# Kernel optimization log

Measured on AMD Instinct MI355X. Metric: run time of the kernel, lower is better.

Reference implementation:

```python
import jax, jax.numpy as jnp
import numpy as np

SIZE, NC, BITS = 16, 3, 8
NV = NC * BITS * SIZE * SIZE  # 6144
NH = NV
N = 32
K_LS = 32   # fixed cap on T=0 local-search Gibbs sweeps (converged rows are fixed points)
K_CP = 16   # fixed cap on coupling MH iterations (converged rows masked out)


def float2bit(x, bits=BITS):
    # quantize [0,1) floats to `bits` binary planes, as in float2bit(...).flatten(1)
    q = jnp.clip(jnp.floor(x * (2 ** bits)), 0, 2 ** bits - 1).astype(jnp.int32)
    shifts = jnp.arange(bits, dtype=jnp.int32)
    b = (q[..., None] >> shifts) & 1  # [N,nc,H,W,bits]
    return b.astype(jnp.float32)


def energy(params, v, h0, h1):
    W0, W1, b0, b1, b2 = params
    e = -jnp.sum(v * b0, axis=1)
    e = e - jnp.sum(h0 * (v @ W0.T + b1), axis=1)
    e = e - jnp.sum(h1 * (h0 @ W1.T + b2), axis=1)
    return e


def _samp(logits, r, T):
    if T == 0:
        return (logits >= 0).astype(jnp.float32)
    return (r < jax.nn.sigmoid(logits / T)).astype(jnp.float32)


def gibbs_step(params, v, h0, h1, even, fix_v, T, key):
    W0, W1, b0, b1, b2 = params
    if T == 0:
        rv = rh0 = rh1 = None
    else:
        kv, k0, k1 = jax.random.split(key, 3)
        rv = jax.random.uniform(kv, v.shape)
        rh0 = jax.random.uniform(k0, h0.shape)
        rh1 = jax.random.uniform(k1, h1.shape)
    # 'even' sweep order: v -> odd h layers -> even h layers
    v_e = v if fix_v else _samp(h0 @ W0 + b0, rv, T)
    h1_e = _samp(h0 @ W1.T + b2, rh1, T)
    h0_e = _samp(v_e @ W0.T + b1 + h1_e @ W1, rh0, T)
    # 'odd' sweep order: even h layers -> v -> odd h layers
    h0_o = _samp(v @ W0.T + b1 + h1 @ W1, rh0, T)
    v_o = v if fix_v else _samp(h0_o @ W0 + b0, rv, T)
    h1_o = _samp(h0_o @ W1.T + b2, rh1, T)
    m = even[:, None]
    return (jnp.where(m, v_e, v_o), jnp.where(m, h0_e, h0_o), jnp.where(m, h1_e, h1_o))


def local_search(params, v, h0, h1, fix_v, key):
    # T=0 deterministic descent with a fixed per-row even/odd split (rand_u drawn once);
    # converged rows are fixed points of the map, so running a fixed K_LS sweeps over the
    # full batch is equivalent to the torch masked while-loop (up to the iteration cap).
    even = jax.random.uniform(key, (v.shape[0],)) < 0.5
    def body(i, s):
        return gibbs_step(params, s[0], s[1], s[2], even, fix_v, 0, None)
    return jax.lax.fori_loop(0, K_LS, body, (v, h0, h1))


def mh_step(params, v, h0, h1, fix_v, key):
    kv, k0, k1, ku = jax.random.split(key, 4)
    v_p = v if fix_v else (jax.random.uniform(kv, v.shape) < 0.5).astype(jnp.float32)
    h0_p = (jax.random.uniform(k0, h0.shape) < 0.5).astype(jnp.float32)
    h1_p = (jax.random.uniform(k1, h1.shape) < 0.5).astype(jnp.float32)
    log_ratio = energy(params, v, h0, h1) - energy(params, v_p, h0_p, h1_p)
    acc = jax.random.uniform(ku, (v.shape[0],)) < jnp.exp(jnp.minimum(log_ratio, 0.0))
    a = acc[:, None]
    return (v if fix_v else jnp.where(a, v_p, v), jnp.where(a, h0_p, h0), jnp.where(a, h1_p, h1))


def _conv_mask(v_new, h0_new, h1_new, v, h0, h1, fix_v):
    c = jnp.ones(v.shape[0], bool) if fix_v else jnp.all(v_new == v, axis=1)
    return c & jnp.all(h0_new == h0, axis=1) & jnp.all(h1_new == h1, axis=1)


def coupling(params, v, h0, h1, fix_v, key):
    k0, key = jax.random.split(key)
    v1, h01, h11 = mh_step(params, v, h0, h1, fix_v, k0)
    e = energy(params, v1, h01, h11)
    conv = _conv_mask(v1, h01, h11, v, h0, h1, fix_v)
    def body(state, k):
        v, h0, h1, e, conv = state
        v2, h02, h12 = mh_step(params, v, h0, h1, fix_v, k)
        de = energy(params, v2, h02, h12) - energy(params, v, h0, h1)
        m = ~conv
        e = e + jnp.where(m, de, 0.0)
        conv2 = _conv_mask(v2, h02, h12, v, h0, h1, fix_v)
        mm = m[:, None]
        v = jnp.where(mm, v2, v)
        h0 = jnp.where(mm, h02, h0)
        h1 = jnp.where(mm, h12, h1)
        return (v, h0, h1, e, conv | conv2), None
    keys = jax.random.split(key, K_CP)
    (v, h0, h1, e, conv), _ = jax.lax.scan(body, (v1, h01, h11, e, conv), keys)
    return e, v, h0, h1


def _dbm_loss(v_img, W0, W1, b0, b1, b2):
    params = (W0, W1, b0, b1, b2)
    n = v_img.shape[0]
    ks = jax.random.split(jax.random.key(42), 13)
    v = float2bit(v_img).reshape(n, -1)
    # positive phase (visibles clamped, fix_v=True)
    h0 = (jax.random.uniform(ks[0], (n, NH)) < 0.5).astype(jnp.float32)
    h1 = (jax.random.uniform(ks[1], (n, NH)) < 0.5).astype(jnp.float32)
    v, h0, h1 = local_search(params, v, h0, h1, True, ks[2])
    even = jax.random.uniform(ks[3], (n,)) < 0.5
    v, h0, h1 = gibbs_step(params, v, h0, h1, even, True, 1, ks[4])
    e_pos, v, h0, h1 = coupling(params, v, h0, h1, True, ks[5])
    # negative phase (free-running)
    v = (jax.random.uniform(ks[6], v.shape) < 0.5).astype(jnp.float32)
    h0 = (jax.random.uniform(ks[7], (n, NH)) < 0.5).astype(jnp.float32)
    h1 = (jax.random.uniform(ks[8], (n, NH)) < 0.5).astype(jnp.float32)
    v, h0, h1 = local_search(params, v, h0, h1, False, ks[9])
    even = jax.random.uniform(ks[10], (n,)) < 0.5
    v, h0, h1 = gibbs_step(params, v, h0, h1, even, False, 1, ks[11])
    e_neg, v, h0, h1 = coupling(params, v, h0, h1, False, ks[12])
    return e_pos - e_neg  # [N]


def setup_inputs() -> dict:
    key = jax.random.key(0)
    kv, kw0, kw1 = jax.random.split(key, 3)
    v = jax.random.uniform(kv, (N, NC, SIZE, SIZE), dtype=jnp.float32)
    # orthogonal-like scale (unit-norm rows): entries ~ 1/sqrt(fan_in)
    W0 = jax.random.normal(kw0, (NH, NV), dtype=jnp.float32) / np.sqrt(NV)
    W1 = jax.random.normal(kw1, (NH, NH), dtype=jnp.float32) / np.sqrt(NH)
    b0 = jnp.zeros((NV,), jnp.float32)
    b1 = jnp.zeros((NH,), jnp.float32)
    b2 = jnp.zeros((NH,), jnp.float32)
    return {"v": v, "W0": W0, "W1": W1, "b0": b0, "b1": b1, "b2": b2}


def reference(v, W0, W1, b0, b1, b2):
    return _dbm_loss(v, W0, W1, b0, b1, b2)
```

## Files before the change

### kernel.cpp

```cpp
#include <hip/hip_runtime.h>
#include <cstdint>
#include <math.h>

typedef unsigned int u32;
typedef unsigned long long u64;
typedef double d4 __attribute__((ext_vector_type(4)));

#define TF_PARTITIONABLE 1

#define NU 6144
#define NB 32
#define NTOT (NU * NB)
#define NWORD 96
#define NCH 8
#define CHK 768
#define NT_TILES 24
#define HALF_BIG 98304u
#define HALF_SMALL 16u

struct Key { u32 a, b; };
struct UVec { float u[NB]; };

__host__ __device__ __forceinline__ void tf2x32(u32 k0, u32 k1, u32 x0, u32 x1, u32& o0, u32& o1) {
  const u32 k2 = k0 ^ k1 ^ 0x1BD11BDAu;
#define TFR(r) { x0 += x1; x1 = (x1 << r) | (x1 >> (32 - r)); x1 ^= x0; }
  x0 += k0; x1 += k1;
  TFR(13) TFR(15) TFR(26) TFR(6)  x0 += k1; x1 += k2 + 1u;
  TFR(17) TFR(29) TFR(16) TFR(24) x0 += k2; x1 += k0 + 2u;
  TFR(13) TFR(15) TFR(26) TFR(6)  x0 += k0; x1 += k1 + 3u;
  TFR(17) TFR(29) TFR(16) TFR(24) x0 += k1; x1 += k2 + 4u;
  TFR(13) TFR(15) TFR(26) TFR(6)  x0 += k2; x1 += k0 + 5u;
#undef TFR
  o0 = x0; o1 = x1;
}

__host__ __device__ __forceinline__ u32 rbits(u32 k0, u32 k1, u32 t, u32 half) {
#if TF_PARTITIONABLE
  (void)half;
  u32 a, b; tf2x32(k0, k1, 0u, t, a, b); return a ^ b;
#else
  u32 a, b;
  if (t < half) { tf2x32(k0, k1, t, half + t, a, b); return a; }
  tf2x32(k0, k1, t - half, t, a, b); return b;
#endif
}

__host__ __device__ __forceinline__ float u01f(u32 bits) {
  union { u32 u; float f; } c; c.u = (bits >> 9) | 0x3f800000u;
  return c.f - 1.0f;
}

__device__ __forceinline__ double pav(int probe, int l) {
  return probe ? (double)(((l * 13 + 5) & 63) + 1) : (double)(l + 1);
}
__device__ __forceinline__ double pbv(int probe, int l) {
  return probe ? (double)(((l * 11 + 2) & 63) + 1) : (double)(((l * 7 + 3) & 63) + 1);
}

__global__ __launch_bounds__(64) void k_calib(int* __restrict__ tbl) {
  int L = threadIdx.x;
  d4 z = {0.0, 0.0, 0.0, 0.0};
  d4 o0 = __builtin_amdgcn_mfma_f64_16x16x4f64(pav(0, L), pbv(0, L), z, 0, 0, 0);
  d4 o1 = __builtin_amdgcn_mfma_f64_16x16x4f64(pav(1, L), pbv(1, L), z, 0, 0, 0);
  int q = L >> 4, m16 = L & 15;
  int best = -1;
  for (int combo = 0; combo < 16; ++combo) {
    int fa = combo & 1, fb = (combo >> 1) & 1, fd = combo >> 2;
    int ok = 1;
    for (int probe = 0; probe < 2; ++probe) {
#pragma unroll
      for (int r = 0; r < 4; ++r) {
        int i, j;
        if (fd == 0)      { j = m16; i = 4 * q + r; }
        else if (fd == 1) { j = m16; i = q + 4 * r; }
        else if (fd == 2) { i = m16; j = 4 * q + r; }
        else              { i = m16; j = q + 4 * r; }
        double pred = 0.0;
#pragma unroll
        for (int k = 0; k < 4; ++k) {
          int la = fa ? (i * 4 + k) : (k * 16 + i);
          int lb = fb ? (j * 4 + k) : (k * 16 + j);
          pred += pav(probe, la) * pbv(probe, lb);
        }
        double obs = probe ? (r == 0 ? o1[0] : r == 1 ? o1[1] : r == 2 ? o1[2] : o1[3])
                           : (r == 0 ? o0[0] : r == 1 ? o0[1] : r == 2 ? o0[2] : o0[3]);
        if (pred != obs) ok = 0;
      }
    }
    if (__all(ok) && best < 0) best = combo;
  }
  int mA = 0, kA = 0, nB = 0, kB = 0, b0_ = 0, bs = 0, j0 = 0, js = 0, okf = 0;
  if (best >= 0) {
    int fa = best & 1, fb = (best >> 1) & 1, fd = best >> 2;
    if (fa) { mA = L >> 2; kA = L & 3; } else { mA = m16; kA = q; }
    if (fb) { nB = L >> 2; kB = L & 3; } else { nB = m16; kB = q; }
    if (fd == 0)      { j0 = m16; js = 0; b0_ = 4 * q; bs = 1; }
    else if (fd == 1) { j0 = m16; js = 0; b0_ = q; bs = 4; }
    else if (fd == 2) { b0_ = m16; bs = 0; j0 = 4 * q; js = 1; }
    else              { b0_ = m16; bs = 0; j0 = q; js = 4; }
    okf = 1;
  }
  int* p = tbl + L * 16;
  p[0] = mA; p[1] = kA; p[2] = nB; p[3] = kB;
  p[4] = b0_; p[5] = bs; p[6] = j0; p[7] = js; p[8] = okf;
}

__global__ void k_init(u32* __restrict__ flag, u32* __restrict__ chg) { *flag = 0u; *chg = 0u; }

__global__ void k_conv(u32* __restrict__ flag, u32* __restrict__ chg) {
  if (*flag == 0u && *chg == 0u) *flag = 1u;
  *chg = 0u;
}

__global__ void k_allconv(const u32* __restrict__ conv, u32* __restrict__ skipc) {
  if (*skipc) return;
  u32 all = 1u;
  for (int b = 0; b < NB; ++b) all &= conv[b];
  if (all) *skipc = 1u;
}

__global__ __launch_bounds__(256) void k_pos_v(const float* __restrict__ vin,
                                               double* __restrict__ xf, u64* __restrict__ pk) {
  int tid = blockIdx.x * 256 + threadIdx.x;
  int b = tid / 768, p = tid % 768;
  float x = vin[tid];
  int q = (int)floorf(x * 256.0f);
  q = q < 0 ? 0 : (q > 255 ? 255 : q);
  ((unsigned char*)pk)[b * 768 + p] = (unsigned char)q;
  int ubase = p * 8;
#pragma unroll
  for (int bit = 0; bit < 8; ++bit)
    xf[(size_t)(ubase + bit) * NB + b] = (double)((q >> bit) & 1);
}

__global__ __launch_bounds__(256) void k_bern(u32 k0, u32 k1,
                                              double* __restrict__ xf, u64* __restrict__ pk,
                                              const u32* __restrict__ skip) {
  if (skip && *skip) return;
  int tid = blockIdx.x * 256 + threadIdx.x;
  int b = tid / NU, j = tid % NU;
  float u = u01f(rbits(k0, k1, (u32)tid, HALF_BIG));
  bool s = u < 0.5f;
  u64 m = __ballot(s);
  if ((threadIdx.x & 63) == 0) pk[tid >> 6] = m;
  xf[(size_t)j * NB + b] = s ? 1.0 : 0.0;
}

__device__ __forceinline__ bool samp_dec(float f, int t1, u32 k0, u32 k1, u32 tid) {
  if (t1) {
    double u = (double)u01f(rbits(k0, k1, tid, HALF_BIG));
    return u < 1.0 / (1.0 + exp(-(double)f));
  }
  return f >= 0.0f;
}

__global__ __launch_bounds__(256) void k_samp(const float* __restrict__ fE, const float* __restrict__ fO,
                                              u32 even, int t1, u32 k0, u32 k1,
                                              double* __restrict__ xf, u64* __restrict__ pk,
                                              const u32* __restrict__ skip, u32* __restrict__ chg) {
  if (skip && *skip) return;
  int tid = blockIdx.x * 256 + threadIdx.x;
  int b = tid / NU, j = tid % NU;
  float f = ((even >> b) & 1u) ? fE[tid] : fO[tid];
  bool s = samp_dec(f, t1, k0, k1, (u32)tid);
  u64 m = __ballot(s);
  if ((threadIdx.x & 63) == 0) {
    int widx = tid >> 6;
    if (chg) { u64 old = pk[widx]; if (old != m) *chg = 1u; }
    pk[widx] = m;
  }
  xf[(size_t)j * NB + b] = s ? 1.0 : 0.0;
}

__global__ __launch_bounds__(256) void k_gemm_n(const float* __restrict__ W, const double* __restrict__ xf,
                                                double* __restrict__ part, const u32* __restrict__ skip,
                                                const int* __restrict__ tbl) {
  if (skip && *skip) return;
  __shared__ float  lw[2][32][69];
  __shared__ double lx[2][32][34];
  int jt = blockIdx.x % 96, c = blockIdx.x / 96;
  int wid = threadIdx.x >> 6, lane = threadIdx.x & 63;
  int kbase = c * CHK;
  int jn0 = jt * 64;
  const int* tp = tbl + lane * 16;
  int okf = tp[8];
  if (okf) {
    int mA = tp[0], kA = tp[1], nB = tp[2], kB = tp[3];
    int bD0 = tp[4], bDs = tp[5], jD0 = tp[6], jDs = tp[7];
    int t256 = threadIdx.x;
    d4 acc0 = {0.0, 0.0, 0.0, 0.0};
    d4 acc1 = {0.0, 0.0, 0.0, 0.0};
#pragma unroll
    for (int r = 0; r < 2; ++r) {
      int idx = r * 256 + t256, kk = idx >> 4, qq = idx & 15;
      double2 xv = *(const double2*)(xf + (size_t)(kbase + kk) * NB + 2 * qq);
      lx[0][kk][2 * qq] = xv.x; lx[0][kk][2 * qq + 1] = xv.y;
      float4 wv4 = *(const float4*)(W + (size_t)(kbase + kk) * NU + jn0 + 4 * qq);
      lw[0][kk][4 * qq + 0] = wv4.x; lw[0][kk][4 * qq + 1] = wv4.y;
      lw[0][kk][4 * qq + 2] = wv4.z; lw[0][kk][4 * qq + 3] = wv4.w;
    }
    __syncthreads();
    int buf = 0;
    for (int t = 0; t < NT_TILES; ++t) {
      double2 x0p, x1p; float4 w0p, w1p;
      bool pf = (t + 1) < NT_TILES;
      if (pf) {
        int k0n = kbase + (t + 1) * 32;
        { int idx = t256,       kk = idx >> 4, qq = idx & 15;
          x0p = *(const double2*)(xf + (size_t)(k0n + kk) * NB + 2 * qq);
          w0p = *(const float4*)(W + (size_t)(k0n + kk) * NU + jn0 + 4 * qq); }
        { int idx = 256 + t256, kk = idx >> 4, qq = idx & 15;
          x1p = *(const double2*)(xf + (size_t)(k0n + kk) * NB + 2 * qq);
          w1p = *(const float4*)(W + (size_t)(k0n + kk) * NU + jn0 + 4 * qq); }
      }
      const float*  lwp = &lw[buf][kB][wid * 16 + nB];
      const double* lxp = &lx[buf][kA][mA];
#pragma unroll
      for (int u = 0; u < 8; ++u) {
        double a0 = lxp[136 * u], a1 = lxp[136 * u + 16];
        double wv = (double)lwp[276 * u];
        acc0 = __builtin_amdgcn_mfma_f64_16x16x4f64(a0, wv, acc0, 0, 0, 0);
        acc1 = __builtin_amdgcn_mfma_f64_16x16x4f64(a1, wv, acc1, 0, 0, 0);
      }
      if (pf) {
        int nb = buf ^ 1;
        { int idx = t256,       kk = idx >> 4, qq = idx & 15;
          lx[nb][kk][2 * qq] = x0p.x; lx[nb][kk][2 * qq + 1] = x0p.y;
          lw[nb][kk][4 * qq + 0] = w0p.x; lw[nb][kk][4 * qq + 1] = w0p.y;
          lw[nb][kk][4 * qq + 2] = w0p.z; lw[nb][kk][4 * qq + 3] = w0p.w; }
        { int idx = 256 + t256, kk = idx >> 4, qq = idx & 15;
          lx[nb][kk][2 * qq] = x1p.x; lx[nb][kk][2 * qq + 1] = x1p.y;
          lw[nb][kk][4 * qq + 0] = w1p.x; lw[nb][kk][4 * qq + 1] = w1p.y;
          lw[nb][kk][4 * qq + 2] = w1p.z; lw[nb][kk][4 * qq + 3] = w1p.w; }
      }
      __syncthreads();
      buf ^= 1;
    }
    int jn = jn0 + wid * 16;
    double* pp = part + (size_t)c * NTOT + jn;
#pragma unroll
    for (int r = 0; r < 4; ++r) {
      int bi = bD0 + bDs * r, jj = jD0 + jDs * r;
      pp[(size_t)bi * NU + jj] = acc0[r];
      pp[(size_t)(bi + 16) * NU + jj] = acc1[r];
    }
  } else {
    double* red = (double*)lx;
    int j = jn0 + lane;
    int i0 = kbase + wid * 192;
    const float* wp = W + (size_t)i0 * NU + j;
    const double* xp = xf + (size_t)i0 * NB;
    double acc[32];
#pragma unroll
    for (int b = 0; b < 32; ++b) acc[b] = 0.0;
    for (int i = 0; i < 192; ++i) {
      double w = (double)wp[(size_t)i * NU];
      const double* xq = xp + (size_t)i * NB;
#pragma unroll
      for (int b = 0; b < 32; ++b) acc[b] = fma(xq[b], w, acc[b]);
    }
    for (int w = 1; w < 4; ++w) {
      if (wid == w) {
#pragma unroll
        for (int b = 0; b < 32; ++b) red[b * 64 + lane] = acc[b];
      }
      __syncthreads();
      if (wid == 0) {
#pragma unroll
        for (int b = 0; b < 32; ++b) acc[b] += red[b * 64 + lane];
      }
      __syncthreads();
    }
    if (wid == 0) {
      double* pp = part + (size_t)c * NTOT + j;
#pragma unroll
      for (int b = 0; b < 32; ++b) pp[(size_t)b * NU] = acc[b];
    }
  }
}

__global__ __launch_bounds__(256) void k_gemm_t(const float* __restrict__ W, const double* __restrict__ xf,
                                                double* __restrict__ part, const u32* __restrict__ skip,
                                                const int* __restrict__ tbl) {
  if (skip && *skip) return;
  __shared__ float  lw[2][32][69];
  __shared__ double lx[2][32][34];
  int jt = blockIdx.x % 96, c = blockIdx.x / 96;
  int wid = threadIdx.x >> 6, lane = threadIdx.x & 63;
  int kbase = c * CHK;
  int jn0 = jt * 64;
  const int* tp = tbl + lane * 16;
  int okf = tp[8];
  if (okf) {
    int mA = tp[0], kA = tp[1], nB = tp[2], kB = tp[3];
    int bD0 = tp[4], bDs = tp[5], jD0 = tp[6], jDs = tp[7];
    int t256 = threadIdx.x;
    d4 acc0 = {0.0, 0.0, 0.0, 0.0};
    d4 acc1 = {0.0, 0.0, 0.0, 0.0};
#pragma unroll
    for (int r = 0; r < 2; ++r) {
      int idx = r * 256 + t256;
      int kk = idx >> 4, qq = idx & 15;
      double2 xv = *(const double2*)(xf + (size_t)(kbase + kk) * NB + 2 * qq);
      lx[0][kk][2 * qq] = xv.x; lx[0][kk][2 * qq + 1] = xv.y;
      int jj = idx >> 3, kq = idx & 7;
      float4 wv4 = *(const float4*)(W + (size_t)(jn0 + jj) * NU + kbase + 4 * kq);
      lw[0][4 * kq + 0][jj] = wv4.x; lw[0][4 * kq + 1][jj] = wv4.y;
      lw[0][4 * kq + 2][jj] = wv4.z; lw[0][4 * kq + 3][jj] = wv4.w;
    }
    __syncthreads();
    int buf = 0;
    for (int t = 0; t < NT_TILES; ++t) {
      double2 x0p, x1p; float4 w0p, w1p;
      bool pf = (t + 1) < NT_TILES;
      if (pf) {
        int k0n = kbase + (t + 1) * 32;
        { int idx = t256,       kk = idx >> 4, qq = idx & 15;
          x0p = *(const double2*)(xf + (size_t)(k0n + kk) * NB + 2 * qq);
          int jj = idx >> 3, kq = idx & 7;
          w0p = *(const float4*)(W + (size_t)(jn0 + jj) * NU + k0n + 4 * kq); }
        { int idx = 256 + t256, kk = idx >> 4, qq = idx & 15;
          x1p = *(const double2*)(xf + (size_t)(k0n + kk) * NB + 2 * qq);
          int jj = idx >> 3, kq = idx & 7;
          w1p = *(const float4*)(W + (size_t)(jn0 + jj) * NU + k0n + 4 * kq); }
      }
      const float*  lwp = &lw[buf][kB][wid * 16 + nB];
      const double* lxp = &lx[buf][kA][mA];
#pragma unroll
      for (int u = 0; u < 8; ++u) {
        double a0 = lxp[136 * u], a1 = lxp[136 * u + 16];
        double wv = (double)lwp[276 * u];
        acc0 = __builtin_amdgcn_mfma_f64_16x16x4f64(a0, wv, acc0, 0, 0, 0);
        acc1 = __builtin_amdgcn_mfma_f64_16x16x4f64(a1, wv, acc1, 0, 0, 0);
      }
      if (pf) {
        int nb = buf ^ 1;
        { int idx = t256,       kk = idx >> 4, qq = idx & 15;
          lx[nb][kk][2 * qq] = x0p.x; lx[nb][kk][2 * qq + 1] = x0p.y;
          int jj = idx >> 3, kq = idx & 7;
          lw[nb][4 * kq + 0][jj] = w0p.x; lw[nb][4 * kq + 1][jj] = w0p.y;
          lw[nb][4 * kq + 2][jj] = w0p.z; lw[nb][4 * kq + 3][jj] = w0p.w; }
        { int idx = 256 + t256, kk = idx >> 4, qq = idx & 15;
          lx[nb][kk][2 * qq] = x1p.x; lx[nb][kk][2 * qq + 1] = x1p.y;
          int jj = idx >> 3, kq = idx & 7;
          lw[nb][4 * kq + 0][jj] = w1p.x; lw[nb][4 * kq + 1][jj] = w1p.y;
          lw[nb][4 * kq + 2][jj] = w1p.z; lw[nb][4 * kq + 3][jj] = w1p.w; }
      }
      __syncthreads();
      buf ^= 1;
    }
    int jn = jn0 + wid * 16;
    double* pp = part + (size_t)c * NTOT + jn;
#pragma unroll
    for (int r = 0; r < 4; ++r) {
      int bi = bD0 + bDs * r, jj = jD0 + jDs * r;
      pp[(size_t)bi * NU + jj] = acc0[r];
      pp[(size_t)(bi + 16) * NU + jj] = acc1[r];
    }
  } else {
    float* lwf = (float*)lw;
    double* red = (double*)lx;
    int qf = threadIdx.x & 7, af = threadIdx.x >> 3;
    double acc[32];
#pragma unroll
    for (int b = 0; b < 32; ++b) acc[b] = 0.0;
    for (int s = 0; s < 24; ++s) {
      int ib = kbase + s * 32;
#pragma unroll
      for (int pass = 0; pass < 2; ++pass) {
        int r = pass * 32 + af;
        float4 w4 = *(const float4*)(W + (size_t)(jn0 + r) * NU + ib + qf * 4);
        lwf[(qf * 4 + 0) * 65 + r] = w4.x;
        lwf[(qf * 4 + 1) * 65 + r] = w4.y;
        lwf[(qf * 4 + 2) * 65 + r] = w4.z;
        lwf[(qf * 4 + 3) * 65 + r] = w4.w;
      }
      __syncthreads();
      int iw = wid * 8;
      for (int ii = 0; ii < 8; ++ii) {
        double w = (double)lwf[(iw + ii) * 65 + lane];
        const double* xq = xf + (size_t)(ib + iw + ii) * NB;
#pragma unroll
        for (int b = 0; b < 32; ++b) acc[b] = fma(xq[b], w, acc[b]);
      }
      __syncthreads();
    }
    for (int w = 1; w < 4; ++w) {
      if (wid == w) {
#pragma unroll
        for (int b = 0; b < 32; ++b) red[b * 64 + lane] = acc[b];
      }
      __syncthreads();
      if (wid == 0) {
#pragma unroll
        for (int b = 0; b < 32; ++b) acc[b] += red[b * 64 + lane];
      }
      __syncthreads();
    }
    if (wid == 0) {
      double* pp = part + (size_t)c * NTOT + jn0 + lane;
#pragma unroll
      for (int b = 0; b < 32; ++b) pp[(size_t)b * NU] = acc[b];
    }
  }
}

__global__ __launch_bounds__(256) void k_reduce(const double* __restrict__ part, const float* __restrict__ bias,
                                                const float* __restrict__ src, float* __restrict__ out,
                                                const u32* __restrict__ skip) {
  if (skip && *skip) return;
  int tid = blockIdx.x * 256 + threadIdx.x;
  int j = tid % NU;
  double s = src ? (double)src[tid] : 0.0;
  if (bias) s += (double)bias[j];
#pragma unroll
  for (int c = 0; c < NCH; ++c) s += part[(size_t)c * NTOT + tid];
  out[tid] = (float)s;
}

__global__ __launch_bounds__(256) void k_redsamp(const double* __restrict__ part, const float* __restrict__ bias,
                                                 const float* __restrict__ src, float* __restrict__ out,
                                                 int t1, u32 k0, u32 k1,
                                                 double* __restrict__ xf, u64* __restrict__ pk,
                                                 const u32* __restrict__ skip, u32 wmask,
                                                 u32* __restrict__ chg) {
  if (skip && *skip) return;
  int tid = blockIdx.x * 256 + threadIdx.x;
  int j = tid % NU, b = tid / NU;
  double s = src ? (double)src[tid] : 0.0;
  if (bias) s += (double)bias[j];
#pragma unroll
  for (int c = 0; c < NCH; ++c) s += part[(size_t)c * NTOT + tid];
  float f = (float)s;
  out[tid] = f;
  bool wr = (wmask >> b) & 1u;
  bool smp = samp_dec(f, t1, k0, k1, (u32)tid);
  u64 m = __ballot(smp);
  if (((threadIdx.x & 63) == 0) && wr) {
    int widx = tid >> 6;
    if (chg) { u64 old = pk[widx]; if (old != m) *chg = 1u; }
    pk[widx] = m;
  }
  if (wr) xf[(size_t)j * NB + b] = smp ? 1.0 : 0.0;
}

__global__ __launch_bounds__(256) void k_energy(const u64* __restrict__ pkv, const u64* __restrict__ pkh0,
                                                const u64* __restrict__ pkh1, const float* __restrict__ f1,
                                                const float* __restrict__ f2, const float* __restrict__ b0,
                                                float* __restrict__ eout, const u32* __restrict__ skip) {
  if (skip && *skip) return;
  __shared__ double red[256];
  int b = blockIdx.x, t = threadIdx.x;
  double s = 0.0;
  for (int j = t; j < NU; j += 256) {
    int w = j >> 6, bit = j & 63;
    if ((pkv [b * NWORD + w] >> bit) & 1ull) s += (double)b0[j];
    if ((pkh0[b * NWORD + w] >> bit) & 1ull) s += (double)f1[(size_t)b * NU + j];
    if ((pkh1[b * NWORD + w] >> bit) & 1ull) s += (double)f2[(size_t)b * NU + j];
  }
  red[t] = s; __syncthreads();
  for (int off = 128; off > 0; off >>= 1) { if (t < off) red[t] += red[t + off]; __syncthreads(); }
  if (t == 0) eout[b] = (float)(-red[0]);
}

__global__ __launch_bounds__(64) void k_accept(float* __restrict__ ecur, const float* __restrict__ eprop,
                                               float* __restrict__ erun, u32* __restrict__ conv,
                                               u32* __restrict__ accf,
                                               const u64* __restrict__ pv, const u64* __restrict__ pcv,
                                               const u64* __restrict__ ph0, const u64* __restrict__ pch0,
                                               const u64* __restrict__ ph1, const u64* __restrict__ pch1,
                                               UVec uv, int first, const u32* __restrict__ skip) {
  if (skip && *skip) return;
  int b = blockIdx.x, t = threadIdx.x;
  u64 diff = 0ull;
  for (int w = t; w < NWORD; w += 64) {
    size_t o = (size_t)b * NWORD + w;
    if (pv) diff |= pv[o] ^ pcv[o];
    diff |= ph0[o] ^ pch0[o];
    diff |= ph1[o] ^ pch1[o];
  }
  int neq = __any(diff != 0ull);
  if (t == 0) {
    float ec = ecur[b], ep = eprop[b];
    bool acc = (double)uv.u[b] < exp(fmin((double)ec - (double)ep, 0.0));
    bool m = first ? true : (conv[b] == 0u);
    bool upd = m && acc;
    if (first) erun[b] = acc ? ep : ec;
    else if (upd) erun[b] += (ep - ec);
    if (upd) ecur[b] = ep;
    u32 c2 = acc ? (neq ? 0u : 1u) : 1u;
    conv[b] = first ? c2 : (conv[b] | c2);
    accf[b] = upd ? 1u : 0u;
  }
}

__global__ __launch_bounds__(256) void k_merge_xf(const u32* __restrict__ accf,
                                                  const u64* __restrict__ pa, u64* __restrict__ ca,
                                                  const u64* __restrict__ pb, u64* __restrict__ cb,
                                                  const u64* __restrict__ pc, u64* __restrict__ cc,
                                                  const u32* __restrict__ skip) {
  if (skip && *skip) return;
  int tid = blockIdx.x * 256 + threadIdx.x;
  int b = tid & 31;
  if (accf[b]) {
    ca[tid] = pa[tid];
    cb[tid] = pb[tid];
    if (pc) cc[tid] = pc[tid];
  }
}

__global__ __launch_bounds__(256) void k_merge_pk(const u32* __restrict__ accf,
                                                  const u64* __restrict__ pa, u64* __restrict__ ca,
                                                  const u64* __restrict__ pb, u64* __restrict__ cb,
                                                  const u64* __restrict__ pc, u64* __restrict__ cc,
                                                  const u32* __restrict__ skip) {
  if (skip && *skip) return;
  int w = blockIdx.x * 256 + threadIdx.x;
  if (w >= NB * NWORD) return;
  int b = w / NWORD;
  if (accf[b]) {
    ca[w] = pa[w];
    cb[w] = pb[w];
    if (pc) cc[w] = pc[w];
  }
}

__global__ void k_final(const float* __restrict__ ep, const float* __restrict__ en, float* __restrict__ out) {
  int b = threadIdx.x;
  if (b < NB) out[b] = ep[b] - en[b];
}

static void split_keys(Key k, int n, Key* out) {
#if TF_PARTITIONABLE
  for (int i = 0; i < n; ++i) { u32 a, b; tf2x32(k.a, k.b, 0u, (u32)i, a, b); out[i].a = a; out[i].b = b; }
#else
  u32 flat[64];
  for (int i = 0; i < n; ++i) { u32 a, b; tf2x32(k.a, k.b, (u32)i, (u32)(n + i), a, b); flat[i] = a; flat[n + i] = b; }
  for (int i = 0; i < n; ++i) { out[i].a = flat[2 * i]; out[i].b = flat[2 * i + 1]; }
#endif
}
static u32 mask32(Key k) {
  u32 m = 0;
  for (int b = 0; b < NB; ++b)
    if (u01f(rbits(k.a, k.b, (u32)b, HALF_SMALL)) < 0.5f) m |= (1u << b);
  return m;
}

extern "C" void kernel_launch(void* const* d_in, const int* in_sizes, int n_in,
                              void* d_out, int out_size, void* d_ws, size_t ws_size,
                              hipStream_t stream) {
  const float* vin = (const float*)d_in[0];
  const float* W0  = (const float*)d_in[1];
  const float* W1  = (const float*)d_in[2];
  const float* b0  = (const float*)d_in[3];
  const float* b1  = (const float*)d_in[4];
  const float* b2  = (const float*)d_in[5];
  float* outp = (float*)d_out;

  char* ws = (char*)d_ws;
  size_t off = 0;
  auto alloc = [&](size_t bytes) -> void* {
    void* p = ws + off; off += (bytes + 255) & ~(size_t)255; return p;
  };
  enum { SV = 0, SH0, SH1, SVE, SH1E, SH0O, SVP, SH0P, SH1P, NS };
  enum { IV = 0, IA, IB, IC, ID, IE, IF2, IP1, IP2, IC2, NF };
  double* XF[NS]; u64* PK[NS]; float* F[NF];
  for (int s = 0; s < NS; ++s) XF[s] = (double*)alloc((size_t)NTOT * 8);
  for (int f = 0; f < NF; ++f) F[f]  = (float*)alloc((size_t)NTOT * 4);
  double* PART = (double*)alloc((size_t)NCH * NTOT * 8);
  for (int s = 0; s < NS; ++s) PK[s] = (u64*)alloc((size_t)NB * NWORD * 8);
  int*   TBL    = (int*)alloc(64 * 16 * 4);
  float* E_CUR  = (float*)alloc(256);
  float* E_PROP = (float*)alloc(256);
  float* E_POS  = (float*)alloc(256);
  float* E_NEG  = (float*)alloc(256);
  u32*   ACC    = (u32*)alloc(256);
  u32*   CONV   = (u32*)alloc(256);
  u32*   FLAG   = (u32*)alloc(256);
  u32*   CHG    = (u32*)alloc(256);
  u32*   SKIPC  = (u32*)alloc(256);
  u32*   DUMMY  = (u32*)alloc(256);
  if (off > ws_size) return;

  Key root{0u, 42u};
  Key ks[13]; split_keys(root, 13, ks);
  const Key KZ{0u, 0u};

  k_calib<<<dim3(1), dim3(64), 0, stream>>>(TBL);

  auto GEMM_T = [&](const float* Wm, int xs, const u32* skip) {
    k_gemm_t<<<dim3(96 * NCH), dim3(256), 0, stream>>>(Wm, XF[xs], PART, skip, TBL);
  };
  auto GEMM_N = [&](const float* Wm, int xs, const u32* skip) {
    k_gemm_n<<<dim3(96 * NCH), dim3(256), 0, stream>>>(Wm, XF[xs], PART, skip, TBL);
  };
  auto RED = [&](const float* bias, const float* src, float* dst, const u32* skip) {
    k_reduce<<<dim3(768), dim3(256), 0, stream>>>(PART, bias, src, dst, skip);
  };
  auto REDS = [&](const float* bias, const float* src, float* dst, int t1, Key k, int sdst,
                  const u32* skip, u32 wm, u32* chg) {
    k_redsamp<<<dim3(768), dim3(256), 0, stream>>>(PART, bias, src, dst, t1, k.a, k.b,
                                                   XF[sdst], PK[sdst], skip, wm, chg);
  };
  auto GT = [&](const float* Wm, int xs, const float* bias, const float* src, float* dst, const u32* skip) {
    GEMM_T(Wm, xs, skip); RED(bias, src, dst, skip);
  };
  auto GN = [&](const float* Wm, int xs, const float* bias, const float* src, float* dst, const u32* skip) {
    GEMM_N(Wm, xs, skip); RED(bias, src, dst, skip);
  };
  auto GTS = [&](const float* Wm, int xs, const float* bias, const float* src, float* dst,
                 int t1, Key k, int sdst, const u32* skip) {
    GEMM_T(Wm, xs, skip); REDS(bias, src, dst, t1, k, sdst, skip, ~0u, nullptr);
  };
  auto GNS = [&](const float* Wm, int xs, const float* bias, const float* src, float* dst,
                 int t1, Key k, int sdst, const u32* skip) {
    GEMM_N(Wm, xs, skip); REDS(bias, src, dst, t1, k, sdst, skip, ~0u, nullptr);
  };
  auto SAMP = [&](const float* fE, const float* fO, u32 even, int t1, Key k, int dst,
                  const u32* skip, u32* chg) {
    k_samp<<<dim3(768), dim3(256), 0, stream>>>(fE, fO, even, t1, k.a, k.b, XF[dst], PK[dst], skip, chg);
  };
  auto BERN = [&](Key k, int dst, const u32* skip) {
    k_bern<<<dim3(768), dim3(256), 0, stream>>>(k.a, k.b, XF[dst], PK[dst], skip);
  };
  auto ENERGY = [&](int sv, int sh0, int sh1, const float* f1, const float* f2, float* eo, const u32* skip) {
    k_energy<<<dim3(32), dim3(256), 0, stream>>>(PK[sv], PK[sh0], PK[sh1], f1, f2, b0, eo, skip);
  };

  auto ls_fixv = [&](u32 evm) {
    auto X = [&](u32 wm) {
      GEMM_T(W1, SH0, FLAG);
      REDS(b2, nullptr, F[IA], 0, KZ, SH1, FLAG, wm, CHG);
    };
    auto Y = [&]() {
      GEMM_N(W1, SH1, FLAG);
      REDS(nullptr, F[IV], F[IC], 0, KZ, SH0, FLAG, ~0u, CHG);
    };
    k_init<<<dim3(1), dim3(1), 0, stream>>>(FLAG, CHG);
    X(evm);
    for (int i = 0; i < 31; ++i) {
      Y(); X(~0u);
      k_conv<<<dim3(1), dim3(1), 0, stream>>>(FLAG, CHG);
    }
    Y(); X(~evm);
  };
  auto ls_free = [&](u32 evm) {
    auto X = [&](u32 wm) {
      GEMM_N(W0, SH0, FLAG);
      REDS(b0, nullptr, F[IE], 0, KZ, SV, FLAG, wm, CHG);
      GEMM_T(W1, SH0, FLAG);
      REDS(b2, nullptr, F[IA], 0, KZ, SH1, FLAG, wm, CHG);
    };
    auto Y = [&]() {
      GT(W0, SV, b1, nullptr, F[IC], FLAG);
      GEMM_N(W1, SH1, FLAG);
      REDS(nullptr, F[IC], F[IC], 0, KZ, SH0, FLAG, ~0u, CHG);
    };
    k_init<<<dim3(1), dim3(1), 0, stream>>>(FLAG, CHG);
    X(evm);
    for (int i = 0; i < 31; ++i) {
      Y(); X(~0u);
      k_conv<<<dim3(1), dim3(1), 0, stream>>>(FLAG, CHG);
    }
    Y(); X(~evm);
  };

  auto gibbs_fixv = [&](u32 even, Key kh0, Key kh1) {
    GTS(W1, SH0, b2, nullptr, F[IA], 1, kh1, SH1E, nullptr);
    GN(W1, SH1E, nullptr, F[IV], F[IB], nullptr);
    GNS(W1, SH1, nullptr, F[IV], F[IC], 1, kh0, SH0O, nullptr);
    GT(W1, SH0O, b2, nullptr, F[ID], nullptr);
    SAMP(F[IB], F[IC], even, 1, kh0, SH0, nullptr, nullptr);
    SAMP(F[IA], F[ID], even, 1, kh1, SH1, nullptr, nullptr);
  };
  auto gibbs_free = [&](u32 even, Key kv, Key kh0, Key kh1) {
    GNS(W0, SH0, b0, nullptr, F[IE], 1, kv, SVE, nullptr);
    GTS(W1, SH0, b2, nullptr, F[IA], 1, kh1, SH1E, nullptr);
    GT(W0, SVE, b1, nullptr, F[IB], nullptr);
    GN(W1, SH1E, nullptr, F[IB], F[IB], nullptr);
    GT(W0, SV, b1, nullptr, F[IC], nullptr);
    GNS(W1, SH1, nullptr, F[IC], F[IC], 1, kh0, SH0O, nullptr);
    GN(W0, SH0O, b0, nullptr, F[IF2], nullptr);
    GT(W1, SH0O, b2, nullptr, F[ID], nullptr);
    SAMP(F[IE], F[IF2], even, 1, kv, SV, nullptr, nullptr);
    SAMP(F[IB], F[IC], even, 1, kh0, SH0, nullptr, nullptr);
    SAMP(F[IA], F[ID], even, 1, kh1, SH1, nullptr, nullptr);
  };

  auto coupling = [&](bool fixv, Key ck, float* erun) {
    Key top[2]; split_keys(ck, 2, top);
    Key cks[17]; cks[0] = top[0];
    { Key rest[16]; split_keys(top[1], 16, rest); for (int i = 0; i < 16; ++i) cks[i + 1] = rest[i]; }
    k_init<<<dim3(1), dim3(1), 0, stream>>>(SKIPC, DUMMY);
    for (int it = 0; it < 17; ++it) {
      const u32* sk = (it == 0) ? nullptr : SKIPC;
      Key sub[4]; split_keys(cks[it], 4, sub);
      UVec uv;
      for (int b = 0; b < NB; ++b) uv.u[b] = u01f(rbits(sub[3].a, sub[3].b, (u32)b, HALF_SMALL));
      if (!fixv) BERN(sub[0], SVP, sk);
      BERN(sub[1], SH0P, sk);
      BERN(sub[2], SH1P, sk);
      const float* f1;
      if (fixv) f1 = F[IV];
      else { GT(W0, SVP, b1, nullptr, F[IP1], sk); f1 = F[IP1]; }
      GT(W1, SH0P, b2, nullptr, F[IP2], sk);
      ENERGY(fixv ? SV : SVP, SH0P, SH1P, f1, F[IP2], E_PROP, sk);
      k_accept<<<dim3(32), dim3(64), 0, stream>>>(E_CUR, E_PROP, erun, CONV, ACC,
          fixv ? nullptr : PK[SVP], fixv ? nullptr : PK[SV],
          PK[SH0P], PK[SH0], PK[SH1P], PK[SH1], uv, it == 0 ? 1 : 0, sk);
      k_merge_xf<<<dim3(768), dim3(256), 0, stream>>>(ACC,
          (const u64*)XF[SH0P], (u64*)XF[SH0], (const u64*)XF[SH1P], (u64*)XF[SH1],
          fixv ? nullptr : (const u64*)XF[SVP], fixv ? nullptr : (u64*)XF[SV], sk);
      k_merge_pk<<<dim3(12), dim3(256), 0, stream>>>(ACC, PK[SH0P], PK[SH0], PK[SH1P], PK[SH1],
          fixv ? nullptr : PK[SVP], fixv ? nullptr : PK[SV], sk);
      k_allconv<<<dim3(1), dim3(1), 0, stream>>>(CONV, SKIPC);
    }
  };

  k_pos_v<<<dim3(96), dim3(256), 0, stream>>>(vin, XF[SV], PK[SV]);
  BERN(ks[0], SH0, nullptr);
  BERN(ks[1], SH1, nullptr);
  GT(W0, SV, b1, nullptr, F[IV], nullptr);
  u32 ev_ls_pos = mask32(ks[2]);
  ls_fixv(ev_ls_pos);
  u32 ev2_pos = mask32(ks[3]);
  Key g4[3]; split_keys(ks[4], 3, g4);
  gibbs_fixv(ev2_pos, g4[1], g4[2]);
  GT(W1, SH0, b2, nullptr, F[IC2], nullptr);
  ENERGY(SV, SH0, SH1, F[IV], F[IC2], E_CUR, nullptr);
  coupling(true, ks[5], E_POS);

  BERN(ks[6], SV, nullptr);
  BERN(ks[7], SH0, nullptr);
  BERN(ks[8], SH1, nullptr);
  u32 ev_ls_neg = mask32(ks[9]);
  ls_free(ev_ls_neg);
  u32 ev2_neg = mask32(ks[10]);
  Key g11[3]; split_keys(ks[11], 3, g11);
  gibbs_free(ev2_neg, g11[0], g11[1], g11[2]);
  GT(W0, SV, b1, nullptr, F[IB], nullptr);
  GT(W1, SH0, b2, nullptr, F[IA], nullptr);
  ENERGY(SV, SH0, SH1, F[IB], F[IA], E_CUR, nullptr);
  coupling(false, ks[12], E_NEG);

  k_final<<<dim3(1), dim3(64), 0, stream>>>(E_POS, E_NEG, outp);
}
```

Baseline: 13.50 ms.

## Split GEMM K into more chunks and read activations directly from global

The K dimension of both GEMM kernels is split into 12 chunks of 512 instead of 8 of 768, which raises the block count for better CU occupancy but adds more partial sums to reduce. The activation operand is no longer staged in shared memory; each lane loads its MFMA A-operand straight from global (cache-resident) memory, so only the weight tile is double-buffered in LDS with a repadded layout. Float scratch buffers are also consolidated to shrink the workspace.

```diff
diff --git a/kernel.cpp b/kernel.cpp
--- a/kernel.cpp
+++ b/kernel.cpp
@@ -12,9 +12,9 @@
 #define NB 32
 #define NTOT (NU * NB)
 #define NWORD 96
-#define NCH 8
-#define CHK 768
-#define NT_TILES 24
+#define NCH 12
+#define CHK 512
+#define NT_TILES 16
 #define HALF_BIG 98304u
 #define HALF_SMALL 16u
 
@@ -176,8 +176,7 @@
                                                 double* __restrict__ part, const u32* __restrict__ skip,
                                                 const int* __restrict__ tbl) {
   if (skip && *skip) return;
-  __shared__ float  lw[2][32][69];
-  __shared__ double lx[2][32][34];
+  __shared__ double smem_d[2560];
   int jt = blockIdx.x % 96, c = blockIdx.x / 96;
   int wid = threadIdx.x >> 6, lane = threadIdx.x & 63;
   int kbase = c * CHK;
@@ -185,6 +184,7 @@
   const int* tp = tbl + lane * 16;
   int okf = tp[8];
   if (okf) {
+    float* lw = (float*)smem_d;
     int mA = tp[0], kA = tp[1], nB = tp[2], kB = tp[3];
     int bD0 = tp[4], bDs = tp[5], jD0 = tp[6], jDs = tp[7];
     int t256 = threadIdx.x;
@@ -193,45 +193,41 @@
 #pragma unroll
     for (int r = 0; r < 2; ++r) {
       int idx = r * 256 + t256, kk = idx >> 4, qq = idx & 15;
-      double2 xv = *(const double2*)(xf + (size_t)(kbase + kk) * NB + 2 * qq);
-      lx[0][kk][2 * qq] = xv.x; lx[0][kk][2 * qq + 1] = xv.y;
-      float4 wv4 = *(const float4*)(W + (size_t)(kbase + kk) * NU + jn0 + 4 * qq);
-      lw[0][kk][4 * qq + 0] = wv4.x; lw[0][kk][4 * qq + 1] = wv4.y;
-      lw[0][kk][4 * qq + 2] = wv4.z; lw[0][kk][4 * qq + 3] = wv4.w;
+      float4 w4 = *(const float4*)(W + (size_t)(kbase + kk) * NU + jn0 + 4 * qq);
+      float* d = &lw[kk * 80 + 4 * qq];
+      d[0] = w4.x; d[1] = w4.y; d[2] = w4.z; d[3] = w4.w;
     }
     __syncthreads();
+    const double* xa = xf + (size_t)(kbase + kA) * NB + mA;
     int buf = 0;
     for (int t = 0; t < NT_TILES; ++t) {
-      double2 x0p, x1p; float4 w0p, w1p;
+      float4 w0p, w1p;
       bool pf = (t + 1) < NT_TILES;
       if (pf) {
         int k0n = kbase + (t + 1) * 32;
         { int idx = t256,       kk = idx >> 4, qq = idx & 15;
-          x0p = *(const double2*)(xf + (size_t)(k0n + kk) * NB + 2 * qq);
           w0p = *(const float4*)(W + (size_t)(k0n + kk) * NU + jn0 + 4 * qq); }
         { int idx = 256 + t256, kk = idx >> 4, qq = idx & 15;
-          x1p = *(const double2*)(xf + (size_t)(k0n + kk) * NB + 2 * qq);
           w1p = *(const float4*)(W + (size_t)(k0n + kk) * NU + jn0 + 4 * qq); }
       }
-      const float*  lwp = &lw[buf][kB][wid * 16 + nB];
-      const double* lxp = &lx[buf][kA][mA];
+      const float* lwp = &lw[(buf * 32 + kB) * 80 + wid * 16 + nB];
+      const double* xt = xa + (size_t)t * 32 * NB;
 #pragma unroll
       for (int u = 0; u < 8; ++u) {
-        double a0 = lxp[136 * u], a1 = lxp[136 * u + 16];
-        double wv = (double)lwp[276 * u];
+        double a0 = xt[u * 4 * NB];
+        double a1 = xt[u * 4 * NB + 16];
+        double wv = (double)lwp[320 * u];
         acc0 = __builtin_amdgcn_mfma_f64_16x16x4f64(a0, wv, acc0, 0, 0, 0);
         acc1 = __builtin_amdgcn_mfma_f64_16x16x4f64(a1, wv, acc1, 0, 0, 0);
       }
       if (pf) {
         int nb = buf ^ 1;
         { int idx = t256,       kk = idx >> 4, qq = idx & 15;
-          lx[nb][kk][2 * qq] = x0p.x; lx[nb][kk][2 * qq + 1] = x0p.y;
-          lw[nb][kk][4 * qq + 0] = w0p.x; lw[nb][kk][4 * qq + 1] = w0p.y;
-          lw[nb][kk][4 * qq + 2] = w0p.z; lw[nb][kk][4 * qq + 3] = w0p.w; }
+          float* d = &lw[(nb * 32 + kk) * 80 + 4 * qq];
+          d[0] = w0p.x; d[1] = w0p.y; d[2] = w0p.z; d[3] = w0p.w; }
         { int idx = 256 + t256, kk = idx >> 4, qq = idx & 15;
-          lx[nb][kk][2 * qq] = x1p.x; lx[nb][kk][2 * qq + 1] = x1p.y;
-          lw[nb][kk][4 * qq + 0] = w1p.x; lw[nb][kk][4 * qq + 1] = w1p.y;
-          lw[nb][kk][4 * qq + 2] = w1p.z; lw[nb][kk][4 * qq + 3] = w1p.w; }
+          float* d = &lw[(nb * 32 + kk) * 80 + 4 * qq];
+          d[0] = w1p.x; d[1] = w1p.y; d[2] = w1p.z; d[3] = w1p.w; }
       }
       __syncthreads();
       buf ^= 1;
@@ -245,15 +241,15 @@
       pp[(size_t)(bi + 16) * NU + jj] = acc1[r];
     }
   } else {
-    double* red = (double*)lx;
+    double* red = smem_d;
     int j = jn0 + lane;
-    int i0 = kbase + wid * 192;
+    int i0 = kbase + wid * 128;
     const float* wp = W + (size_t)i0 * NU + j;
     const double* xp = xf + (size_t)i0 * NB;
     double acc[32];
 #pragma unroll
     for (int b = 0; b < 32; ++b) acc[b] = 0.0;
-    for (int i = 0; i < 192; ++i) {
+    for (int i = 0; i < 128; ++i) {
       double w = (double)wp[(size_t)i * NU];
       const double* xq = xp + (size_t)i * NB;
 #pragma unroll
@@ -283,8 +279,7 @@
                                                 double* __restrict__ part, const u32* __restrict__ skip,
                                                 const int* __restrict__ tbl) {
   if (skip && *skip) return;
-  __shared__ float  lw[2][32][69];
-  __shared__ double lx[2][32][34];
+  __shared__ double smem_d[2176];
   int jt = blockIdx.x % 96, c = blockIdx.x / 96;
   int wid = threadIdx.x >> 6, lane = threadIdx.x & 63;
   int kbase = c * CHK;
@@ -292,6 +287,7 @@
   const int* tp = tbl + lane * 16;
   int okf = tp[8];
   if (okf) {
+    float* lw = (float*)smem_d;
     int mA = tp[0], kA = tp[1], nB = tp[2], kB = tp[3];
     int bD0 = tp[4], bDs = tp[5], jD0 = tp[6], jDs = tp[7];
     int t256 = threadIdx.x;
@@ -299,52 +295,42 @@
     d4 acc1 = {0.0, 0.0, 0.0, 0.0};
 #pragma unroll
     for (int r = 0; r < 2; ++r) {
-      int idx = r * 256 + t256;
-      int kk = idx >> 4, qq = idx & 15;
-      double2 xv = *(const double2*)(xf + (size_t)(kbase + kk) * NB + 2 * qq);
-      lx[0][kk][2 * qq] = xv.x; lx[0][kk][2 * qq + 1] = xv.y;
-      int jj = idx >> 3, kq = idx & 7;
-      float4 wv4 = *(const float4*)(W + (size_t)(jn0 + jj) * NU + kbase + 4 * kq);
-      lw[0][4 * kq + 0][jj] = wv4.x; lw[0][4 * kq + 1][jj] = wv4.y;
-      lw[0][4 * kq + 2][jj] = wv4.z; lw[0][4 * kq + 3][jj] = wv4.w;
+      int idx = r * 256 + t256, jj = idx >> 3, kq = idx & 7;
+      float4 w4 = *(const float4*)(W + (size_t)(jn0 + jj) * NU + kbase + 4 * kq);
+      float* d = &lw[jj * 34 + 4 * kq];
+      d[0] = w4.x; d[1] = w4.y; d[2] = w4.z; d[3] = w4.w;
     }
     __syncthreads();
+    const double* xa = xf + (size_t)(kbase + kA) * NB + mA;
     int buf = 0;
     for (int t = 0; t < NT_TILES; ++t) {
-      double2 x0p, x1p; float4 w0p, w1p;
+      float4 w0p, w1p;
       bool pf = (t + 1) < NT_TILES;
       if (pf) {
         int k0n = kbase + (t + 1) * 32;
-        { int idx = t256,       kk = idx >> 4, qq = idx & 15;
-          x0p = *(const double2*)(xf + (size_t)(k0n + kk) * NB + 2 * qq);
-          int jj = idx >> 3, kq = idx & 7;
+        { int idx = t256,       jj = idx >> 3, kq = idx & 7;
           w0p = *(const float4*)(W + (size_t)(jn0 + jj) * NU + k0n + 4 * kq); }
-        { int idx = 256 + t256, kk = idx >> 4, qq = idx & 15;
-          x1p = *(const double2*)(xf + (size_t)(k0n + kk) * NB + 2 * qq);
-          int jj = idx >> 3, kq = idx & 7;
+        { int idx = 256 + t256, jj = idx >> 3, kq = idx & 7;
           w1p = *(const float4*)(W + (size_t)(jn0 + jj) * NU + k0n + 4 * kq); }
       }
-      const float*  lwp = &lw[buf][kB][wid * 16 + nB];
-      const double* lxp = &lx[buf][kA][mA];
+      const float* lwp = &lw[(buf * 64 + wid * 16 + nB) * 34 + kB];
+      const double* xt = xa + (size_t)t * 32 * NB;
 #pragma unroll
       for (int u = 0; u < 8; ++u) {
-        double a0 = lxp[136 * u], a1 = lxp[136 * u + 16];
-        double wv = (double)lwp[276 * u];
+        double a0 = xt[u * 4 * NB];
+        double a1 = xt[u * 4 * NB + 16];
+        double wv = (double)lwp[4 * u];
         acc0 = __builtin_amdgcn_mfma_f64_16x16x4f64(a0, wv, acc0, 0, 0, 0);
         acc1 = __builtin_amdgcn_mfma_f64_16x16x4f64(a1, wv, acc1, 0, 0, 0);
       }
       if (pf) {
         int nb = buf ^ 1;
-        { int idx = t256,       kk = idx >> 4, qq = idx & 15;
-          lx[nb][kk][2 * qq] = x0p.x; lx[nb][kk][2 * qq + 1] = x0p.y;
-          int jj = idx >> 3, kq = idx & 7;
-          lw[nb][4 * kq + 0][jj] = w0p.x; lw[nb][4 * kq + 1][jj] = w0p.y;
-          lw[nb][4 * kq + 2][jj] = w0p.z; lw[nb][4 * kq + 3][jj] = w0p.w; }
-        { int idx = 256 + t256, kk = idx >> 4, qq = idx & 15;
-          lx[nb][kk][2 * qq] = x1p.x; lx[nb][kk][2 * qq + 1] = x1p.y;
-          int jj = idx >> 3, kq = idx & 7;
-          lw[nb][4 * kq + 0][jj] = w1p.x; lw[nb][4 * kq + 1][jj] = w1p.y;
-          lw[nb][4 * kq + 2][jj] = w1p.z; lw[nb][4 * kq + 3][jj] = w1p.w; }
+        { int idx = t256,       jj = idx >> 3, kq = idx & 7;
+          float* d = &lw[(nb * 64 + jj) * 34 + 4 * kq];
+          d[0] = w0p.x; d[1] = w0p.y; d[2] = w0p.z; d[3] = w0p.w; }
+        { int idx = 256 + t256, jj = idx >> 3, kq = idx & 7;
+          float* d = &lw[(nb * 64 + jj) * 34 + 4 * kq];
+          d[0] = w1p.x; d[1] = w1p.y; d[2] = w1p.z; d[3] = w1p.w; }
       }
       __syncthreads();
       buf ^= 1;
@@ -358,13 +344,13 @@
       pp[(size_t)(bi + 16) * NU + jj] = acc1[r];
     }
   } else {
-    float* lwf = (float*)lw;
-    double* red = (double*)lx;
+    float* lwf = (float*)smem_d;
+    double* red = smem_d;
     int qf = threadIdx.x & 7, af = threadIdx.x >> 3;
     double acc[32];
 #pragma unroll
     for (int b = 0; b < 32; ++b) acc[b] = 0.0;
-    for (int s = 0; s < 24; ++s) {
+    for (int s = 0; s < NT_TILES; ++s) {
       int ib = kbase + s * 32;
 #pragma unroll
       for (int pass = 0; pass < 2; ++pass) {
@@ -563,7 +549,7 @@
     void* p = ws + off; off += (bytes + 255) & ~(size_t)255; return p;
   };
   enum { SV = 0, SH0, SH1, SVE, SH1E, SH0O, SVP, SH0P, SH1P, NS };
-  enum { IV = 0, IA, IB, IC, ID, IE, IF2, IP1, IP2, IC2, NF };
+  enum { IV = 0, IA, IB, IC, ID, IE, IF2, NF };
   double* XF[NS]; u64* PK[NS]; float* F[NF];
   for (int s = 0; s < NS; ++s) XF[s] = (double*)alloc((size_t)NTOT * 8);
   for (int f = 0; f < NF; ++f) F[f]  = (float*)alloc((size_t)NTOT * 4);
@@ -702,9 +688,9 @@
       BERN(sub[2], SH1P, sk);
       const float* f1;
       if (fixv) f1 = F[IV];
-      else { GT(W0, SVP, b1, nullptr, F[IP1], sk); f1 = F[IP1]; }
-      GT(W1, SH0P, b2, nullptr, F[IP2], sk);
-      ENERGY(fixv ? SV : SVP, SH0P, SH1P, f1, F[IP2], E_PROP, sk);
+      else { GT(W0, SVP, b1, nullptr, F[IC], sk); f1 = F[IC]; }
+      GT(W1, SH0P, b2, nullptr, F[ID], sk);
+      ENERGY(fixv ? SV : SVP, SH0P, SH1P, f1, F[ID], E_PROP, sk);
       k_accept<<<dim3(32), dim3(64), 0, stream>>>(E_CUR, E_PROP, erun, CONV, ACC,
           fixv ? nullptr : PK[SVP], fixv ? nullptr : PK[SV],
           PK[SH0P], PK[SH0], PK[SH1P], PK[SH1], uv, it == 0 ? 1 : 0, sk);
@@ -726,8 +712,8 @@
   u32 ev2_pos = mask32(ks[3]);
   Key g4[3]; split_keys(ks[4], 3, g4);
   gibbs_fixv(ev2_pos, g4[1], g4[2]);
-  GT(W1, SH0, b2, nullptr, F[IC2], nullptr);
-  ENERGY(SV, SH0, SH1, F[IV], F[IC2], E_CUR, nullptr);
+  GT(W1, SH0, b2, nullptr, F[ID], nullptr);
+  ENERGY(SV, SH0, SH1, F[IV], F[ID], E_CUR, nullptr);
   coupling(true, ks[5], E_POS);
 
   BERN(ks[6], SV, nullptr);
```

Measured after the change: 15.63 ms. +15.8%, slower.
